# Performance work log

Hardware: AMD Instinct MI355X
Metric: run time of the kernel (lower is better)

The kernel has to match this reference:

```python
import jax, jax.numpy as jnp
import numpy as np

B, T, K = 512, 1024, 48


def setup_inputs() -> dict:
    key = jax.random.key(0)
    k1, k2, k3, k4, k5, k6, k7 = jax.random.split(key, 7)
    emissions = jax.random.normal(k1, (B, T, K), dtype=jnp.float32)
    tags = jax.random.randint(k2, (B, T), 0, K)
    # contiguous prefix mask (lengths in [T//2, T]) as assumed by the CRF
    lengths = jax.random.randint(k3, (B,), T // 2, T + 1)
    mask = jnp.arange(T)[None, :] < lengths[:, None]
    u = lambda k, s: jax.random.uniform(k, s, jnp.float32, -0.1, 0.1)
    return {
        "emissions": emissions,
        "tags": tags,
        "mask": mask,
        "transitions": u(k4, (K, K)),
        "start_transitions": u(k5, (K,)),
        "end_transitions": u(k6, (K,)),
    }


def _log_normalizer(emissions, mask, transitions, start_transitions, end_transitions):
    # emissions: [B,T,K]; forward algorithm over the tag lattice
    score0 = start_transitions + emissions[:, 0]  # [B,K]

    def step(score, xs):
        em_t, m_t = xs  # [B,K], [B]
        # [B,K,1] + [K,K] + [B,1,K] -> logsumexp over prev tag
        nxt = jax.nn.logsumexp(score[:, :, None] + transitions[None] + em_t[:, None, :], axis=1)
        score = jnp.where(m_t[:, None], nxt, score)
        return score, None

    em_tm = jnp.swapaxes(emissions[:, 1:], 0, 1)  # time-major [T-1,B,K]
    mk_tm = jnp.swapaxes(mask[:, 1:], 0, 1)       # [T-1,B]
    score, _ = jax.lax.scan(step, score0, (em_tm, mk_tm))
    return jax.nn.logsumexp(score + end_transitions, axis=1)  # [B]


def _sequence_score(emissions, tags, mask, transitions, start_transitions, end_transitions):
    emit = jnp.take_along_axis(emissions, tags[:, :, None], axis=2)[:, :, 0]  # [B,T]
    trans = transitions[tags[:, :-1], tags[:, 1:]]  # [B,T-1]
    score = start_transitions[tags[:, 0]] + emit[:, 0]
    score = score + jnp.sum((trans + emit[:, 1:]) * mask[:, 1:].astype(emissions.dtype), axis=1)
    last_idx = jnp.sum(mask.astype(jnp.int32), axis=1) - 1  # [B]
    last_tags = jnp.take_along_axis(tags, last_idx[:, None], axis=1)[:, 0]
    return score + end_transitions[last_tags]


def reference(emissions, tags, mask, transitions, start_transitions, end_transitions):
    log_z = _log_normalizer(emissions, mask, transitions, start_transitions, end_transitions)
    seq_score = _sequence_score(emissions, tags, mask, transitions, start_transitions, end_transitions)
    return jnp.mean(log_z - seq_score)
```

## Files before the change

### kernel.cpp

```cpp
#include <hip/hip_runtime.h>
#include <stdint.h>

#define BB 512
#define TT 1024
#define KK 48
#define PF 8

__device__ __forceinline__ int mask_at(const void* m, int idx, bool bytes) {
    return bytes ? (int)(((const uint8_t*)m)[idx] != 0)
                 : (int)(((const int*)m)[idx] != 0);
}

__device__ __forceinline__ float bcast(float v, int lane) {
    return __int_as_float(__builtin_amdgcn_readlane(__float_as_int(v), lane));
}

__global__ __launch_bounds__(64, 1) void crf_fwd(
    const float* __restrict__ em, const int* __restrict__ tags,
    const void* __restrict__ mask, const float* __restrict__ trans,
    const float* __restrict__ start, const float* __restrict__ endt,
    float* __restrict__ ws)
{
    const int b = blockIdx.x;
    const int lane = threadIdx.x;
    const bool active = lane < KK;
    const int j = active ? lane : KK - 1;

    const bool mb = (*(const int*)mask) == 0x01010101;

    int cnt = 0;
    for (int t = lane; t < TT; t += 64) cnt += mask_at(mask, b * TT + t, mb);
    #pragma unroll
    for (int off = 32; off >= 1; off >>= 1) cnt += __shfl_xor(cnt, off);
    const int len = cnt;

    float etr[KK];
    #pragma unroll
    for (int i = 0; i < KK; ++i) {
        etr[i] = active ? __expf(trans[i * KK + j]) : 0.0f;
        asm volatile("" : "+v"(etr[i]));
    }

    const float* emb = em + (size_t)b * TT * KK;

    float s0 = start[j] + emb[j];
    float c = bcast(s0, 0);
    float pcur = active ? __expf(s0 - c) : 0.0f;

    float pipe[PF];
    #pragma unroll
    for (int d = 0; d < PF; ++d) pipe[d] = emb[(1 + d) * KK + j];

    int t = 1;
    while (t + PF <= len) {
        float eexp[PF];
        #pragma unroll
        for (int d = 0; d < PF; ++d) eexp[d] = __expf(pipe[d]);
        #pragma unroll
        for (int d = 0; d < PF; ++d) {
            int tt = t + PF + d; tt = tt < TT ? tt : TT - 1;
            pipe[d] = emb[tt * KK + j];
        }
        #pragma unroll
        for (int d = 0; d < PF; ++d) {
            float s[KK];
            #pragma unroll
            for (int k = 0; k < KK; ++k) s[k] = bcast(pcur, k);
            __builtin_amdgcn_sched_barrier(0);
            float scale = eexp[d];
            const bool renorm = (d == 0) || (d == 4);
            if (renorm) scale *= __builtin_amdgcn_rcpf(s[0]);
            float q0 = s[0] * etr[0];
            float q1 = s[1] * etr[1];
            float q2 = s[2] * etr[2];
            float q3 = s[3] * etr[3];
            #pragma unroll
            for (int k = 4; k < KK; k += 4) {
                q0 = fmaf(s[k],     etr[k],     q0);
                q1 = fmaf(s[k + 1], etr[k + 1], q1);
                q2 = fmaf(s[k + 2], etr[k + 2], q2);
                q3 = fmaf(s[k + 3], etr[k + 3], q3);
            }
            if (renorm) c += __logf(s[0]);
            float qs = (q0 + q1) + (q2 + q3);
            pcur = qs * scale;
        }
        t += PF;
    }
    while (t < len) {
        float e = __expf(pipe[0]);
        #pragma unroll
        for (int d = 0; d < PF - 1; ++d) pipe[d] = pipe[d + 1];
        {
            float s[KK];
            #pragma unroll
            for (int k = 0; k < KK; ++k) s[k] = bcast(pcur, k);
            __builtin_amdgcn_sched_barrier(0);
            float scale = e * __builtin_amdgcn_rcpf(s[0]);
            float q0 = s[0] * etr[0];
            float q1 = s[1] * etr[1];
            float q2 = s[2] * etr[2];
            float q3 = s[3] * etr[3];
            #pragma unroll
            for (int k = 4; k < KK; k += 4) {
                q0 = fmaf(s[k],     etr[k],     q0);
                q1 = fmaf(s[k + 1], etr[k + 1], q1);
                q2 = fmaf(s[k + 2], etr[k + 2], q2);
                q3 = fmaf(s[k + 3], etr[k + 3], q3);
            }
            c += __logf(s[0]);
            float qs = (q0 + q1) + (q2 + q3);
            pcur = qs * scale;
        }
        ++t;
    }

    float v = active ? pcur * __expf(endt[j]) : 0.0f;
    #pragma unroll
    for (int off = 32; off >= 1; off >>= 1) v += __shfl_xor(v, off);

    const int* tgb = tags + b * TT;
    float sq = 0.f;
    for (int tt2 = lane; tt2 < TT; tt2 += 64) {
        if (tt2 >= 1 && tt2 < len) {
            int tp = tgb[tt2 - 1], tc = tgb[tt2];
            sq += trans[tp * KK + tc] + emb[tt2 * KK + tc];
        }
    }
    #pragma unroll
    for (int off = 32; off >= 1; off >>= 1) sq += __shfl_xor(sq, off);

    if (lane == 0) {
        int t0 = tgb[0];
        ws[b]      = c + __logf(v);
        ws[BB + b] = sq + start[t0] + emb[t0] + endt[tgb[len - 1]];
    }
}

__global__ __launch_bounds__(256) void crf_final(const float* __restrict__ ws,
                                                 float* __restrict__ out)
{
    __shared__ float red[256];
    float s = 0.f;
    for (int b = threadIdx.x; b < BB; b += 256) s += ws[b] - ws[BB + b];
    red[threadIdx.x] = s;
    __syncthreads();
    for (int off = 128; off > 0; off >>= 1) {
        if (threadIdx.x < off) red[threadIdx.x] += red[threadIdx.x + off];
        __syncthreads();
    }
    if (threadIdx.x == 0) out[0] = red[0] / (float)BB;
}

extern "C" void kernel_launch(void* const* d_in, const int* in_sizes, int n_in,
                              void* d_out, int out_size, void* d_ws, size_t ws_size,
                              hipStream_t stream) {
    const float* em    = (const float*)d_in[0];
    const int*   tags  = (const int*)d_in[1];
    const void*  mask  = d_in[2];
    const float* trans = (const float*)d_in[3];
    const float* start = (const float*)d_in[4];
    const float* endt  = (const float*)d_in[5];
    float* ws  = (float*)d_ws;
    float* out = (float*)d_out;

    crf_fwd  <<<BB, 64,  0, stream>>>(em, tags, mask, trans, start, endt, ws);
    crf_final<<<1,  256, 0, stream>>>(ws, out);
}
```

Before: 334.2 us.

## Interleave two sequences per wavefront with LDS broadcast and packed FMA

Each 64-lane block now runs the CRF forward recursion for two batch rows, interleaving their independent dependency chains to hide latency. The per-step score broadcast switches from 48 readlane instructions to an LDS store plus float4 reads, and the dot product uses packed two-wide FMA. Every row now runs for the full T steps and captures its result at its own length, so work for shorter sequences is wasted. Launching half as many blocks (256) may leave compute units on the 256-CU device underused and lengthens each block's serial chain.

```diff
diff --git a/kernel.cpp b/kernel.cpp
--- a/kernel.cpp
+++ b/kernel.cpp
@@ -6,6 +6,8 @@
 #define KK 48
 #define PF 8
 
+typedef float v2f __attribute__((ext_vector_type(2)));
+
 __device__ __forceinline__ int mask_at(const void* m, int idx, bool bytes) {
     return bytes ? (int)(((const uint8_t*)m)[idx] != 0)
                  : (int)(((const int*)m)[idx] != 0);
@@ -14,6 +16,8 @@
 __device__ __forceinline__ float bcast(float v, int lane) {
     return __int_as_float(__builtin_amdgcn_readlane(__float_as_int(v), lane));
 }
+
+__device__ __forceinline__ v2f mk2(float x, float y) { v2f r; r.x = x; r.y = y; return r; }
 
 __global__ __launch_bounds__(64, 1) void crf_fwd(
     const float* __restrict__ em, const int* __restrict__ tags,
@@ -21,119 +25,167 @@
     const float* __restrict__ start, const float* __restrict__ endt,
     float* __restrict__ ws)
 {
-    const int b = blockIdx.x;
+    __shared__ __align__(16) float plA[64];
+    __shared__ __align__(16) float plB[64];
+
+    const int bid = blockIdx.x;
+    const int bA = 2 * bid, bB = 2 * bid + 1;
     const int lane = threadIdx.x;
     const bool active = lane < KK;
     const int j = active ? lane : KK - 1;
 
     const bool mb = (*(const int*)mask) == 0x01010101;
 
-    int cnt = 0;
-    for (int t = lane; t < TT; t += 64) cnt += mask_at(mask, b * TT + t, mb);
-    #pragma unroll
-    for (int off = 32; off >= 1; off >>= 1) cnt += __shfl_xor(cnt, off);
-    const int len = cnt;
-
-    float etr[KK];
-    #pragma unroll
-    for (int i = 0; i < KK; ++i) {
-        etr[i] = active ? __expf(trans[i * KK + j]) : 0.0f;
-        asm volatile("" : "+v"(etr[i]));
-    }
-
-    const float* emb = em + (size_t)b * TT * KK;
-
-    float s0 = start[j] + emb[j];
-    float c = bcast(s0, 0);
-    float pcur = active ? __expf(s0 - c) : 0.0f;
-
-    float pipe[PF];
-    #pragma unroll
-    for (int d = 0; d < PF; ++d) pipe[d] = emb[(1 + d) * KK + j];
-
-    int t = 1;
-    while (t + PF <= len) {
-        float eexp[PF];
-        #pragma unroll
-        for (int d = 0; d < PF; ++d) eexp[d] = __expf(pipe[d]);
+    int cntA = 0, cntB = 0;
+    for (int t = lane; t < TT; t += 64) {
+        cntA += mask_at(mask, bA * TT + t, mb);
+        cntB += mask_at(mask, bB * TT + t, mb);
+    }
+    #pragma unroll
+    for (int off = 32; off >= 1; off >>= 1) {
+        cntA += __shfl_xor(cntA, off);
+        cntB += __shfl_xor(cntB, off);
+    }
+    const int lenA = __builtin_amdgcn_readfirstlane(cntA);
+    const int lenB = __builtin_amdgcn_readfirstlane(cntB);
+
+    v2f etr2[KK / 2];
+    #pragma unroll
+    for (int i = 0; i < KK / 2; ++i) {
+        float e0 = active ? __expf(trans[(2 * i)     * KK + j]) : 0.0f;
+        float e1 = active ? __expf(trans[(2 * i + 1) * KK + j]) : 0.0f;
+        v2f t2 = mk2(e0, e1);
+        asm volatile("" : "+v"(t2));
+        etr2[i] = t2;
+    }
+
+    const float* embA = em + (size_t)bA * TT * KK;
+    const float* embB = em + (size_t)bB * TT * KK;
+
+    float s0A = start[j] + embA[j];
+    float s0B = start[j] + embB[j];
+    float cAc = bcast(s0A, 0);
+    float cBc = bcast(s0B, 0);
+    float pA = active ? __expf(s0A - cAc) : 0.0f;
+    float pB = active ? __expf(s0B - cBc) : 0.0f;
+
+    plA[lane] = pA;
+    plB[lane] = pB;
+    asm volatile("" ::: "memory");
+    float4 rA[12], rB[12];
+    const float* plAf = plA;
+    const float* plBf = plB;
+    #pragma unroll
+    for (int i = 0; i < 12; ++i) rA[i] = *(const float4*)(plAf + 4 * i);
+    #pragma unroll
+    for (int i = 0; i < 12; ++i) rB[i] = *(const float4*)(plBf + 4 * i);
+    asm volatile("" ::: "memory");
+
+    float pipeA[PF], pipeB[PF];
+    #pragma unroll
+    for (int d = 0; d < PF; ++d) {
+        pipeA[d] = embA[(size_t)(1 + d) * KK + j];
+        pipeB[d] = embB[(size_t)(1 + d) * KK + j];
+    }
+
+    float pcapA = 0.f, pcapB = 0.f, ccapA = 0.f, ccapB = 0.f;
+
+    for (int t = 1; t + PF <= TT + 1; t += PF) {
+        const bool tailA = (t + PF > lenA);
+        const bool tailB = (t + PF > lenB);
         #pragma unroll
         for (int d = 0; d < PF; ++d) {
-            int tt = t + PF + d; tt = tt < TT ? tt : TT - 1;
-            pipe[d] = emb[tt * KK + j];
+            const int tc = t + d;
+            const bool rn = (d == 0) || (d == 4);
+            if (tc == lenA) { pcapA = pA; ccapA = cAc; }
+            if (tc == lenB) { pcapB = pB; ccapB = cBc; }
+            {
+                float eA = __expf(pipeA[d]);
+                { int tt = tc + PF; tt = tt < TT ? tt : TT - 1;
+                  pipeA[d] = embA[(size_t)tt * KK + j]; }
+                const bool renorm = rn || tailA;
+                float s0 = rA[0].x;
+                float scale = eA;
+                if (renorm) scale *= __builtin_amdgcn_rcpf(s0);
+                v2f Q01 = mk2(rA[0].x, rA[0].y) * etr2[0];
+                v2f Q23 = mk2(rA[0].z, rA[0].w) * etr2[1];
+                #pragma unroll
+                for (int i = 1; i < 12; ++i) {
+                    Q01 = __builtin_elementwise_fma(mk2(rA[i].x, rA[i].y), etr2[2 * i],     Q01);
+                    Q23 = __builtin_elementwise_fma(mk2(rA[i].z, rA[i].w), etr2[2 * i + 1], Q23);
+                }
+                if (renorm) cAc += __logf(s0);
+                float qs = (Q01.x + Q01.y) + (Q23.x + Q23.y);
+                pA = qs * scale;
+                asm volatile("" ::: "memory");
+                plA[lane] = pA;
+                asm volatile("" ::: "memory");
+                #pragma unroll
+                for (int i = 0; i < 12; ++i) rA[i] = *(const float4*)(plAf + 4 * i);
+                asm volatile("" ::: "memory");
+            }
+            {
+                float eB = __expf(pipeB[d]);
+                { int tt = tc + PF; tt = tt < TT ? tt : TT - 1;
+                  pipeB[d] = embB[(size_t)tt * KK + j]; }
+                const bool renorm = rn || tailB;
+                float s0 = rB[0].x;
+                float scale = eB;
+                if (renorm) scale *= __builtin_amdgcn_rcpf(s0);
+                v2f Q01 = mk2(rB[0].x, rB[0].y) * etr2[0];
+                v2f Q23 = mk2(rB[0].z, rB[0].w) * etr2[1];
+                #pragma unroll
+                for (int i = 1; i < 12; ++i) {
+                    Q01 = __builtin_elementwise_fma(mk2(rB[i].x, rB[i].y), etr2[2 * i],     Q01);
+                    Q23 = __builtin_elementwise_fma(mk2(rB[i].z, rB[i].w), etr2[2 * i + 1], Q23);
+                }
+                if (renorm) cBc += __logf(s0);
+                float qs = (Q01.x + Q01.y) + (Q23.x + Q23.y);
+                pB = qs * scale;
+                asm volatile("" ::: "memory");
+                plB[lane] = pB;
+                asm volatile("" ::: "memory");
+                #pragma unroll
+                for (int i = 0; i < 12; ++i) rB[i] = *(const float4*)(plBf + 4 * i);
+                asm volatile("" ::: "memory");
+            }
         }
-        #pragma unroll
-        for (int d = 0; d < PF; ++d) {
-            float s[KK];
-            #pragma unroll
-            for (int k = 0; k < KK; ++k) s[k] = bcast(pcur, k);
-            __builtin_amdgcn_sched_barrier(0);
-            float scale = eexp[d];
-            const bool renorm = (d == 0) || (d == 4);
-            if (renorm) scale *= __builtin_amdgcn_rcpf(s[0]);
-            float q0 = s[0] * etr[0];
-            float q1 = s[1] * etr[1];
-            float q2 = s[2] * etr[2];
-            float q3 = s[3] * etr[3];
-            #pragma unroll
-            for (int k = 4; k < KK; k += 4) {
-                q0 = fmaf(s[k],     etr[k],     q0);
-                q1 = fmaf(s[k + 1], etr[k + 1], q1);
-                q2 = fmaf(s[k + 2], etr[k + 2], q2);
-                q3 = fmaf(s[k + 3], etr[k + 3], q3);
-            }
-            if (renorm) c += __logf(s[0]);
-            float qs = (q0 + q1) + (q2 + q3);
-            pcur = qs * scale;
+    }
+
+    const float ee = active ? __expf(endt[j]) : 0.0f;
+    float vA = pcapA * ee;
+    float vB = pcapB * ee;
+    #pragma unroll
+    for (int off = 32; off >= 1; off >>= 1) {
+        vA += __shfl_xor(vA, off);
+        vB += __shfl_xor(vB, off);
+    }
+
+    const int* tgA = tags + bA * TT;
+    const int* tgB = tags + bB * TT;
+    float sqA = 0.f, sqB = 0.f;
+    for (int tt2 = lane; tt2 < TT; tt2 += 64) {
+        if (tt2 >= 1 && tt2 < lenA) {
+            int tp = tgA[tt2 - 1], tn = tgA[tt2];
+            sqA += trans[tp * KK + tn] + embA[(size_t)tt2 * KK + tn];
         }
-        t += PF;
-    }
-    while (t < len) {
-        float e = __expf(pipe[0]);
-        #pragma unroll
-        for (int d = 0; d < PF - 1; ++d) pipe[d] = pipe[d + 1];
-        {
-            float s[KK];
-            #pragma unroll
-            for (int k = 0; k < KK; ++k) s[k] = bcast(pcur, k);
-            __builtin_amdgcn_sched_barrier(0);
-            float scale = e * __builtin_amdgcn_rcpf(s[0]);
-            float q0 = s[0] * etr[0];
-            float q1 = s[1] * etr[1];
-            float q2 = s[2] * etr[2];
-            float q3 = s[3] * etr[3];
-            #pragma unroll
-            for (int k = 4; k < KK; k += 4) {
-                q0 = fmaf(s[k],     etr[k],     q0);
-                q1 = fmaf(s[k + 1], etr[k + 1], q1);
-                q2 = fmaf(s[k + 2], etr[k + 2], q2);
-                q3 = fmaf(s[k + 3], etr[k + 3], q3);
-            }
-            c += __logf(s[0]);
-            float qs = (q0 + q1) + (q2 + q3);
-            pcur = qs * scale;
+        if (tt2 >= 1 && tt2 < lenB) {
+            int tp = tgB[tt2 - 1], tn = tgB[tt2];
+            sqB += trans[tp * KK + tn] + embB[(size_t)tt2 * KK + tn];
         }
-        ++t;
-    }
-
-    float v = active ? pcur * __expf(endt[j]) : 0.0f;
-    #pragma unroll
-    for (int off = 32; off >= 1; off >>= 1) v += __shfl_xor(v, off);
-
-    const int* tgb = tags + b * TT;
-    float sq = 0.f;
-    for (int tt2 = lane; tt2 < TT; tt2 += 64) {
-        if (tt2 >= 1 && tt2 < len) {
-            int tp = tgb[tt2 - 1], tc = tgb[tt2];
-            sq += trans[tp * KK + tc] + emb[tt2 * KK + tc];
-        }
-    }
-    #pragma unroll
-    for (int off = 32; off >= 1; off >>= 1) sq += __shfl_xor(sq, off);
+    }
+    #pragma unroll
+    for (int off = 32; off >= 1; off >>= 1) {
+        sqA += __shfl_xor(sqA, off);
+        sqB += __shfl_xor(sqB, off);
+    }
 
     if (lane == 0) {
-        int t0 = tgb[0];
-        ws[b]      = c + __logf(v);
-        ws[BB + b] = sq + start[t0] + emb[t0] + endt[tgb[len - 1]];
+        int t0A = tgA[0], t0B = tgB[0];
+        ws[bA]      = ccapA + __logf(vA);
+        ws[BB + bA] = sqA + start[t0A] + embA[t0A] + endt[tgA[lenA - 1]];
+        ws[bB]      = ccapB + __logf(vB);
+        ws[BB + bB] = sqB + start[t0B] + embB[t0B] + endt[tgB[lenB - 1]];
     }
 }
 
@@ -164,6 +216,6 @@
     float* ws  = (float*)d_ws;
     float* out = (float*)d_out;
 
-    crf_fwd  <<<BB, 64,  0, stream>>>(em, tags, mask, trans, start, endt, ws);
-    crf_final<<<1,  256, 0, stream>>>(ws, out);
-}
+    crf_fwd  <<<BB / 2, 64, 0, stream>>>(em, tags, mask, trans, start, endt, ws);
+    crf_final<<<1,      256, 0, stream>>>(ws, out);
+}
```

Result: slower. 483.3 us (+44.6%).

## Split CRF forward matvec across lane groups via LDS and packed FMA

Applied to the files above, without the earlier changes.

Replaces the 48 per-step readlane broadcasts with an LDS round-trip. Each step writes the score vector to shared memory, and four 16-lane groups each read 12 previous-tag scores, do packed two-wide FMAs against pre-exponentiated transitions, then combine partial sums with xor shuffles. The loop now always runs the full sequence length and captures the state at the block's true length, which removes the separate tail loop and its data-dependent trip count. In exchange, every block does extra steps past its length, and each step now pays LDS write/read latency and two cross-lane shuffles on the serial dependency chain.

```diff
diff --git a/kernel.cpp b/kernel.cpp
--- a/kernel.cpp
+++ b/kernel.cpp
@@ -5,6 +5,8 @@
 #define TT 1024
 #define KK 48
 #define PF 8
+
+typedef float v2f __attribute__((ext_vector_type(2)));
 
 __device__ __forceinline__ int mask_at(const void* m, int idx, bool bytes) {
     return bytes ? (int)(((const uint8_t*)m)[idx] != 0)
@@ -15,16 +17,28 @@
     return __int_as_float(__builtin_amdgcn_readlane(__float_as_int(v), lane));
 }
 
+__device__ __forceinline__ v2f mk2(float x, float y) { v2f r; r.x = x; r.y = y; return r; }
+
+__device__ __forceinline__ float xred4(float h) {
+    h += __shfl_xor(h, 16);
+    h += __shfl_xor(h, 32);
+    return h;
+}
+
 __global__ __launch_bounds__(64, 1) void crf_fwd(
     const float* __restrict__ em, const int* __restrict__ tags,
     const void* __restrict__ mask, const float* __restrict__ trans,
     const float* __restrict__ start, const float* __restrict__ endt,
     float* __restrict__ ws)
 {
+    __shared__ __align__(16) float pl[64];
+
     const int b = blockIdx.x;
     const int lane = threadIdx.x;
-    const bool active = lane < KK;
-    const int j = active ? lane : KK - 1;
+    const int g = lane >> 4;
+    const int l = lane & 15;
+    const bool ownj = lane < KK;
+    const int j = ownj ? lane : KK - 1;
 
     const bool mb = (*(const int*)mask) == 0x01010101;
 
@@ -34,88 +48,76 @@
     for (int off = 32; off >= 1; off >>= 1) cnt += __shfl_xor(cnt, off);
     const int len = cnt;
 
-    float etr[KK];
+    v2f etr[6][3];
     #pragma unroll
-    for (int i = 0; i < KK; ++i) {
-        etr[i] = active ? __expf(trans[i * KK + j]) : 0.0f;
-        asm volatile("" : "+v"(etr[i]));
+    for (int mm = 0; mm < 6; ++mm) {
+        #pragma unroll
+        for (int o = 0; o < 3; ++o) {
+            const int i0 = 12 * g + 2 * mm;
+            const int jo = 16 * o + l;
+            v2f t2 = mk2(__expf(trans[i0 * KK + jo]),
+                         __expf(trans[(i0 + 1) * KK + jo]));
+            asm volatile("" : "+v"(t2));
+            etr[mm][o] = t2;
+        }
     }
 
     const float* emb = em + (size_t)b * TT * KK;
 
-    float s0 = start[j] + emb[j];
-    float c = bcast(s0, 0);
-    float pcur = active ? __expf(s0 - c) : 0.0f;
+    float s0i = start[j] + emb[j];
+    float c = bcast(s0i, 0);
+    float psc = ownj ? __expf(s0i - c) : 0.0f;
+
+    pl[lane] = psc;
 
     float pipe[PF];
     #pragma unroll
-    for (int d = 0; d < PF; ++d) pipe[d] = emb[(1 + d) * KK + j];
+    for (int d = 0; d < PF; ++d) pipe[d] = emb[(size_t)(1 + d) * KK + j];
 
-    int t = 1;
-    while (t + PF <= len) {
-        float eexp[PF];
-        #pragma unroll
-        for (int d = 0; d < PF; ++d) eexp[d] = __expf(pipe[d]);
+    const float* grp = pl + 12 * g;
+    const bool selB = (g == 1), selC = (g >= 2);
+    float pcap = 0.f, ccap = 0.f;
+
+    for (int t = 1; t + PF <= TT + 1; t += PF) {
+        const bool tail = (t + PF > len);
         #pragma unroll
         for (int d = 0; d < PF; ++d) {
-            int tt = t + PF + d; tt = tt < TT ? tt : TT - 1;
-            pipe[d] = emb[tt * KK + j];
+            const int tc = t + d;
+            const bool renorm = (d == 0) || (d == 4) || tail;
+            if (tc == len) { pcap = psc; ccap = c; }
+            float e = __expf(pipe[d]);
+            { int tt = tc + PF; tt = tt < TT ? tt : TT - 1;
+              pipe[d] = emb[(size_t)tt * KK + j]; }
+            float4 qa = *(const float4*)(grp);
+            float4 qb = *(const float4*)(grp + 4);
+            float4 qc = *(const float4*)(grp + 8);
+            float s0u = bcast(qa.x, 0);
+            v2f p2[6];
+            p2[0] = mk2(qa.x, qa.y); p2[1] = mk2(qa.z, qa.w);
+            p2[2] = mk2(qb.x, qb.y); p2[3] = mk2(qb.z, qb.w);
+            p2[4] = mk2(qc.x, qc.y); p2[5] = mk2(qc.z, qc.w);
+            v2f A0 = p2[0] * etr[0][0];
+            v2f A1 = p2[0] * etr[0][1];
+            v2f A2 = p2[0] * etr[0][2];
+            #pragma unroll
+            for (int mm = 1; mm < 6; ++mm) {
+                A0 = __builtin_elementwise_fma(p2[mm], etr[mm][0], A0);
+                A1 = __builtin_elementwise_fma(p2[mm], etr[mm][1], A1);
+                A2 = __builtin_elementwise_fma(p2[mm], etr[mm][2], A2);
+            }
+            float h0 = A0.x + A0.y, h1 = A1.x + A1.y, h2 = A2.x + A2.y;
+            float o0 = xred4(h0), o1 = xred4(h1), o2 = xred4(h2);
+            float sel = selB ? o1 : o0;
+            sel       = selC ? o2 : sel;
+            float scale = e;
+            if (renorm) scale *= __builtin_amdgcn_rcpf(s0u);
+            psc = sel * scale;
+            if (renorm) c += __logf(s0u);
+            pl[lane] = psc;
         }
-        #pragma unroll
-        for (int d = 0; d < PF; ++d) {
-            float s[KK];
-            #pragma unroll
-            for (int k = 0; k < KK; ++k) s[k] = bcast(pcur, k);
-            __builtin_amdgcn_sched_barrier(0);
-            float scale = eexp[d];
-            const bool renorm = (d == 0) || (d == 4);
-            if (renorm) scale *= __builtin_amdgcn_rcpf(s[0]);
-            float q0 = s[0] * etr[0];
-            float q1 = s[1] * etr[1];
-            float q2 = s[2] * etr[2];
-            float q3 = s[3] * etr[3];
-            #pragma unroll
-            for (int k = 4; k < KK; k += 4) {
-                q0 = fmaf(s[k],     etr[k],     q0);
-                q1 = fmaf(s[k + 1], etr[k + 1], q1);
-                q2 = fmaf(s[k + 2], etr[k + 2], q2);
-                q3 = fmaf(s[k + 3], etr[k + 3], q3);
-            }
-            if (renorm) c += __logf(s[0]);
-            float qs = (q0 + q1) + (q2 + q3);
-            pcur = qs * scale;
-        }
-        t += PF;
-    }
-    while (t < len) {
-        float e = __expf(pipe[0]);
-        #pragma unroll
-        for (int d = 0; d < PF - 1; ++d) pipe[d] = pipe[d + 1];
-        {
-            float s[KK];
-            #pragma unroll
-            for (int k = 0; k < KK; ++k) s[k] = bcast(pcur, k);
-            __builtin_amdgcn_sched_barrier(0);
-            float scale = e * __builtin_amdgcn_rcpf(s[0]);
-            float q0 = s[0] * etr[0];
-            float q1 = s[1] * etr[1];
-            float q2 = s[2] * etr[2];
-            float q3 = s[3] * etr[3];
-            #pragma unroll
-            for (int k = 4; k < KK; k += 4) {
-                q0 = fmaf(s[k],     etr[k],     q0);
-                q1 = fmaf(s[k + 1], etr[k + 1], q1);
-                q2 = fmaf(s[k + 2], etr[k + 2], q2);
-                q3 = fmaf(s[k + 3], etr[k + 3], q3);
-            }
-            c += __logf(s[0]);
-            float qs = (q0 + q1) + (q2 + q3);
-            pcur = qs * scale;
-        }
-        ++t;
     }
 
-    float v = active ? pcur * __expf(endt[j]) : 0.0f;
+    float v = ownj ? pcap * __expf(endt[j]) : 0.0f;
     #pragma unroll
     for (int off = 32; off >= 1; off >>= 1) v += __shfl_xor(v, off);
 
@@ -123,8 +125,8 @@
     float sq = 0.f;
     for (int tt2 = lane; tt2 < TT; tt2 += 64) {
         if (tt2 >= 1 && tt2 < len) {
-            int tp = tgb[tt2 - 1], tc = tgb[tt2];
-            sq += trans[tp * KK + tc] + emb[tt2 * KK + tc];
+            int tp = tgb[tt2 - 1], tn = tgb[tt2];
+            sq += trans[tp * KK + tn] + emb[(size_t)tt2 * KK + tn];
         }
     }
     #pragma unroll
@@ -132,7 +134,7 @@
 
     if (lane == 0) {
         int t0 = tgb[0];
-        ws[b]      = c + __logf(v);
+        ws[b]      = ccap + __logf(v);
         ws[BB + b] = sq + start[t0] + emb[t0] + endt[tgb[len - 1]];
     }
 }
```

After: 368.6 us. 10.3% more time.
